# Performance work log

Hardware: AMD Instinct MI355X
Metric: run time of the kernel (lower is better)

The kernel has to match this reference:

```python
import jax, jax.numpy as jnp
import numpy as np

H = 8          # num_heads
EPS = 1e-6     # layernorm epsilon
NEG_INF = -1e9


def _ln(x, g, b):
    m = jnp.mean(x, axis=-1, keepdims=True)
    v = jnp.mean(jnp.square(x - m), axis=-1, keepdims=True)
    return g * (x - m) * jax.lax.rsqrt(v + EPS) + b


def _mha(xq, kv, wq, wk, wv, wo, bias):
    # xq: [B,Tq,D], kv: [B,Tk,D]; weights [D,D]. Returns (out [B,Tq,D], weights [B,H,Tq,Tk]).
    B, Tq, D = xq.shape
    dh = D // H
    q = (xq @ wq) * (dh ** -0.5)
    k = kv @ wk
    v = kv @ wv
    q = q.reshape(B, Tq, H, dh).transpose(0, 2, 1, 3)
    k = k.reshape(B, -1, H, dh).transpose(0, 2, 1, 3)
    v = v.reshape(B, -1, H, dh).transpose(0, 2, 1, 3)
    logits = jnp.einsum('bhqd,bhkd->bhqk', q, k)
    if bias is not None:
        logits = logits + bias
    w = jax.nn.softmax(logits, axis=-1)
    out = jnp.einsum('bhqk,bhkd->bhqd', w, v).transpose(0, 2, 1, 3).reshape(B, Tq, D)
    return out @ wo, w


def setup_inputs() -> dict:
    key = jax.random.key(0)
    ks = jax.random.split(key, 16)
    B, Td, Te, D, F, L = 2, 2048, 2048, 512, 2048, 2
    s = 0.02
    inp = {
        'x': jax.random.normal(ks[0], (B, Td, D), jnp.float32),
        'enc_a': jax.random.normal(ks[1], (B, Te, D), jnp.float32),
        'enc_c': jax.random.normal(ks[2], (B, Te, D), jnp.float32),
        'sa_wq': jax.random.normal(ks[3], (L, D, D), jnp.float32) * s,
        'sa_wk': jax.random.normal(ks[4], (L, D, D), jnp.float32) * s,
        'sa_wv': jax.random.normal(ks[5], (L, D, D), jnp.float32) * s,
        'sa_wo': jax.random.normal(ks[6], (L, D, D), jnp.float32) * s,
        'ed_wq': jax.random.normal(ks[7], (L, D, D), jnp.float32) * s,
        'ed_wk': jax.random.normal(ks[8], (L, D, D), jnp.float32) * s,
        'ed_wv': jax.random.normal(ks[9], (L, D, D), jnp.float32) * s,
        'ed_wo': jax.random.normal(ks[10], (L, D, D), jnp.float32) * s,
        'ffn_w1': jax.random.normal(ks[11], (L, D, F), jnp.float32) * s,
        'ffn_w2': jax.random.normal(ks[12], (L, F, D), jnp.float32) * s,
        'ln1_g': jnp.ones((L, D), jnp.float32), 'ln1_b': jnp.zeros((L, D), jnp.float32),
        'ln2_g': jnp.ones((L, D), jnp.float32), 'ln2_b': jnp.zeros((L, D), jnp.float32),
        'ln3_g': jnp.ones((L, D), jnp.float32), 'ln3_b': jnp.zeros((L, D), jnp.float32),
        'out_g': jnp.ones((D,), jnp.float32), 'out_b': jnp.zeros((D,), jnp.float32),
    }
    return inp


def reference(x, enc_a, enc_c, sa_wq, sa_wk, sa_wv, sa_wo, ed_wq, ed_wk, ed_wv, ed_wo,
              ffn_w1, ffn_w2, ln1_g, ln1_b, ln2_g, ln2_b, ln3_g, ln3_b, out_g, out_b):
    B, T, D = x.shape
    L = sa_wq.shape[0]
    # decoder self-attention causal bias, broadcast over [B,H]
    causal = jnp.where(jnp.tril(jnp.ones((T, T), bool)), 0.0, NEG_INF)[None, None]
    avg = None
    for i in range(L):
        h = _ln(x, ln1_g[i], ln1_b[i])
        y, _ = _mha(h, h, sa_wq[i], sa_wk[i], sa_wv[i], sa_wo[i], causal)
        x = x + y  # residual (dropout inactive at eval)
        h = _ln(x, ln2_g[i], ln2_b[i])
        y0, _ = _mha(h, enc_a, ed_wq[i], ed_wk[i], ed_wv[i], ed_wo[i], None)
        y1, w = _mha(h, enc_c, ed_wq[i], ed_wk[i], ed_wv[i], ed_wo[i], None)
        # original overwrites attn_scores with second call's head-averaged weights
        scores = jnp.mean(w, axis=1) / L
        avg = scores if avg is None else avg + scores
        x = x + y0 + y1
        h = _ln(x, ln3_g[i], ln3_b[i])
        x = x + jax.nn.relu(h @ ffn_w1[i]) @ ffn_w2[i]
    x = _ln(x, out_g, out_b)
    return x, avg
```

## Files before the change

kernel.cpp:

```cpp
#include <hip/hip_runtime.h>
#include <hip/hip_bf16.h>

#define BB 2
#define TT 2048
#define DD 512
#define FF 2048
#define HH 8
#define DH 64
#define LL 2
#define MM (BB*TT)

typedef __attribute__((ext_vector_type(8))) short bf16x8;
typedef __attribute__((ext_vector_type(4))) float f32x4;

__device__ __forceinline__ float bf2f(unsigned short u) {
    return __uint_as_float(((unsigned int)u) << 16);
}
__device__ __forceinline__ unsigned short f2bf(float f) {
    unsigned int u = __float_as_uint(f);
    u += 0x7fffu + ((u >> 16) & 1u);
    return (unsigned short)(u >> 16);
}
__device__ __forceinline__ unsigned int cvtpk(float a, float b) {
    unsigned int r;
    asm("v_cvt_pk_bf16_f32 %0, %1, %2" : "=v"(r) : "v"(a), "v"(b));
    return r;
}
__device__ __forceinline__ void gload16(const void* g, void* l) {
    __builtin_amdgcn_global_load_lds((__attribute__((address_space(1))) void*)g,
                                     (__attribute__((address_space(3))) void*)l, 16, 0, 0);
}

template<bool BF16OUT>
__global__ __launch_bounds__(256) void ln_kernel(const float* __restrict__ x,
                                                 const float* __restrict__ g,
                                                 const float* __restrict__ b,
                                                 void* __restrict__ out)
{
    const int row = blockIdx.x;
    const int tid = threadIdx.x;
    const float2 v = ((const float2*)(x + (size_t)row * DD))[tid];
    float s = v.x + v.y;
    float q = v.x * v.x + v.y * v.y;
    #pragma unroll
    for (int off = 32; off; off >>= 1) {
        s += __shfl_down(s, off);
        q += __shfl_down(q, off);
    }
    __shared__ float ss[4], qq[4];
    const int wid = tid >> 6;
    if ((tid & 63) == 0) { ss[wid] = s; qq[wid] = q; }
    __syncthreads();
    s = ss[0] + ss[1] + ss[2] + ss[3];
    q = qq[0] + qq[1] + qq[2] + qq[3];
    const float mean = s * (1.0f / DD);
    const float var = q * (1.0f / DD) - mean * mean;
    const float inv = rsqrtf(var + 1e-6f);
    const float2 gg = ((const float2*)g)[tid];
    const float2 bb = ((const float2*)b)[tid];
    const float ox = gg.x * (v.x - mean) * inv + bb.x;
    const float oy = gg.y * (v.y - mean) * inv + bb.y;
    if (BF16OUT) {
        const unsigned int pk = cvtpk(ox, oy);
        ((unsigned int*)((unsigned short*)out + (size_t)row * DD))[tid] = pk;
    } else {
        float2 o; o.x = ox; o.y = oy;
        ((float2*)((float*)out + (size_t)row * DD))[tid] = o;
    }
}

struct CvtEJob { const float* s; unsigned short* d; };
struct CvtEJobs2 { CvtEJob j[2]; };

__global__ __launch_bounds__(256) void cvt_kernel(CvtEJobs2 P, int n)
{
    const CvtEJob jb = P.j[blockIdx.z];
    const int i = (blockIdx.x * 256 + threadIdx.x) * 8;
    if (i >= n) return;
    const float4 a = *(const float4*)(jb.s + i);
    const float4 b = *(const float4*)(jb.s + i + 4);
    unsigned int o[4];
    o[0] = cvtpk(a.x, a.y); o[1] = cvtpk(a.z, a.w);
    o[2] = cvtpk(b.x, b.y); o[3] = cvtpk(b.z, b.w);
    *(bf16x8*)(jb.d + i) = *(bf16x8*)o;
}

struct CvtTJob { const float* s; unsigned short* d; int K; int N; };
struct CvtTJobs20 { CvtTJob j[20]; };

__global__ __launch_bounds__(256) void cvtT_kernel(CvtTJobs20 P)
{
    __shared__ float t[32][33];
    const CvtTJob jb = P.j[blockIdx.z];
    const int gk = blockIdx.y << 5, gn = blockIdx.x << 5;
    if (gk >= jb.K || gn >= jb.N) return;
    const int tx = threadIdx.x & 31, ty = threadIdx.x >> 5;
    #pragma unroll
    for (int i = 0; i < 4; ++i)
        t[ty + i * 8][tx] = jb.s[(size_t)(gk + ty + i * 8) * jb.N + gn + tx];
    __syncthreads();
    #pragma unroll
    for (int i = 0; i < 4; ++i)
        jb.d[(size_t)(gn + ty + i * 8) * jb.K + gk + tx] = f2bf(t[tx][ty + i * 8]);
}

struct GemmJob {
    const unsigned short* A;
    const unsigned short* Wt;
    const float* res;
    float* Cf;
    unsigned short* Cb;
    unsigned short* Ct;
    float scale;
    int relu;
};
struct GemmJobs8 { GemmJob j[8]; };

__global__ __launch_bounds__(256, 2) void gemm_mfma(GemmJobs8 P, int M, int N, int K)
{
    __shared__ __align__(16) unsigned char lds[32768];
    const GemmJob jb = P.j[blockIdx.z];
    const int tid = threadIdx.x, lane = tid & 63, w = tid >> 6;
    const int bn = blockIdx.x << 7, bm = blockIdx.y << 7;
    const int wr = (w >> 1) << 6, wc = (w & 1) << 6;
    const size_t strA = (size_t)K * 2;

    f32x4 acc[4][4] = {};
    const int akey = (lane & 7) << 4;
    const int frow = lane & 15;
    const int kq = (lane >> 4) << 4;

    for (int kt = 0; kt < K; kt += 64) {
        __syncthreads();
        #pragma unroll
        for (int c = 0; c < 4; ++c) {
            const int q = c * 4 + w;
            const int o = (q << 10) + (lane << 4);
            const int row = o >> 7;
            const int colb = (o & 127) ^ ((row & 7) << 4);
            gload16((const char*)jb.A + (size_t)(bm + row) * strA + kt * 2 + colb,
                    lds + (q << 10));
            gload16((const char*)jb.Wt + (size_t)(bn + row) * strA + kt * 2 + colb,
                    lds + 16384 + (q << 10));
        }
        asm volatile("s_waitcnt vmcnt(0)" ::: "memory");
        __syncthreads();
        #pragma unroll
        for (int kk = 0; kk < 2; ++kk) {
            bf16x8 av[4], bv[4];
            #pragma unroll
            for (int i = 0; i < 4; ++i) {
                const int rA = wr + (i << 4) + frow;
                av[i] = *(const bf16x8*)(lds + (rA << 7) + ((((kk << 6) + kq)) ^ akey));
                const int rB = wc + (i << 4) + frow;
                bv[i] = *(const bf16x8*)(lds + 16384 + (rB << 7) + ((((kk << 6) + kq)) ^ akey));
            }
            #pragma unroll
            for (int i = 0; i < 4; ++i)
                #pragma unroll
                for (int j = 0; j < 4; ++j)
                    acc[i][j] = __builtin_amdgcn_mfma_f32_16x16x32_bf16(av[i], bv[j], acc[i][j], 0, 0, 0);
        }
    }

    const int crow0 = (lane >> 4) << 2;
    const int ccol = lane & 15;
    if (jb.Ct) {
        #pragma unroll
        for (int i = 0; i < 4; ++i)
            #pragma unroll
            for (int j = 0; j < 4; ++j) {
                const int gm = bm + wr + (i << 4) + crow0;
                const int gn = bn + wc + (j << 4) + ccol;
                const int bI = gm >> 11, t = gm & 2047;
                const int hI = gn >> 6, d = gn & 63;
                uint2 pk;
                pk.x = cvtpk(acc[i][j][0], acc[i][j][1]);
                pk.y = cvtpk(acc[i][j][2], acc[i][j][3]);
                *(uint2*)(jb.Ct + ((size_t)((bI * HH + hI) * DH + d)) * TT + t) = pk;
            }
        return;
    }
    #pragma unroll
    for (int i = 0; i < 4; ++i) {
        #pragma unroll
        for (int j = 0; j < 4; ++j) {
            #pragma unroll
            for (int r = 0; r < 4; ++r) {
                const int gm = bm + wr + (i << 4) + crow0 + r;
                const int gn = bn + wc + (j << 4) + ccol;
                float v = acc[i][j][r] * jb.scale;
                if (jb.relu) v = fmaxf(v, 0.f);
                const size_t idx = (size_t)gm * N + gn;
                if (jb.res) v += jb.res[idx];
                if (jb.Cf) jb.Cf[idx] = v;
                if (jb.Cb) jb.Cb[idx] = f2bf(v);
            }
        }
    }
}

template<bool CAUSAL, bool DUAL, int NQ>
__global__ __launch_bounds__(256, (NQ == 1) ? 4 : 3) void flash_mfma(
    const unsigned short* __restrict__ q,
    const unsigned short* __restrict__ ka, const unsigned short* __restrict__ vta,
    const unsigned short* __restrict__ kc, const unsigned short* __restrict__ vtc,
    unsigned short* __restrict__ Opart,
    float* __restrict__ mlpart)
{
    __shared__ __align__(16) char lds[(NQ == 1) ? 40960 : 49152];
    const int tid = threadIdx.x;
    const int lane = tid & 63, w = tid >> 6;
    const int g4 = lane >> 4, c = lane & 15;

    constexpr int GX = (32 / NQ) * 2;
    const int f = blockIdx.x + GX * (blockIdx.y + 8 * blockIdx.z);
    const int xcd = f & 7;
    const int tt = f >> 3;
    const int u = tt % GX;
    const int half = u & 1, jq = u >> 1;
    const int grp = (tt / GX) * 8 + xcd;
    int b, h, which;
    if (DUAL) { which = grp & 1; b = (grp >> 1) & 1; h = grp >> 2; }
    else      { which = 0;       b = grp & 1;        h = grp >> 1; }
    const int q0 = jq * (64 * NQ);
    const int q0w = q0 + w * (16 * NQ);
    const int kendw = q0w + 16 * NQ;

    const unsigned short* k  = (DUAL && which) ? kc : ka;
    const unsigned short* vt = (DUAL && which) ? vtc : vta;
    const int slot = (DUAL ? (which << 1) : 0) + half;
    unsigned short* Od = Opart + (size_t)slot * MM * DD;
    float* mld = mlpart + (size_t)slot * (BB * HH * TT * 2);

    bf16x8 Qf[NQ][2];
    #pragma unroll
    for (int jb = 0; jb < NQ; ++jb) {
        const unsigned short* qp = q + (size_t)(b * TT + q0w + (jb << 4) + c) * DD + h * DH + (g4 << 3);
        Qf[jb][0] = *(const bf16x8*)qp;
        Qf[jb][1] = *(const bf16x8*)(qp + 32);
    }
    const char* kbase = (const char*)(k + (size_t)b * TT * DD + h * DH);
    const char* vtb   = (const char*)(vt + (size_t)(b * HH + h) * DH * TT);
    char* Pw = lds + 32768 + w * (NQ * 2048);
    const int pkey = (c & 7) << 4;

    f32x4 O[NQ][4] = {};
    float mval[NQ], lpart[NQ];
    #pragma unroll
    for (int jb = 0; jb < NQ; ++jb) { mval[jb] = -1e30f; lpart[jb] = 0.f; }

    const int ntt = CAUSAL ? ((q0 + 64 * NQ) >> 6) : (TT >> 6);
    const int tBeg = half ? ((ntt + 1) >> 1) : 0;
    const int tEnd = half ? ntt : ((ntt + 1) >> 1);

    auto STAGE = [&](int t, int sel) {
        const int kt = t << 6;
        char* Kb = lds + sel * 8192;
        char* Vb = lds + 16384 + sel * 8192;
        #pragma unroll
        for (int c8 = 0; c8 < 2; ++c8) {
            const int qc = (c8 << 2) + w;
            const int o = (qc << 10) + (lane << 4);
            const int row = o >> 7;
            const int colb = (o & 127) ^ ((row & 7) << 4);
            gload16(kbase + (size_t)(kt + row) * (DD * 2) + colb, Kb + (qc << 10));
            gload16(vtb + (size_t)row * (TT * 2) + kt * 2 + colb, Vb + (qc << 10));
        }
    };

    if (tBeg < tEnd) {
        STAGE(tBeg, 0);
        asm volatile("s_waitcnt vmcnt(0)" ::: "memory");
        __syncthreads();

        for (int t = tBeg; t < tEnd; ++t) {
            const int cur = (t - tBeg) & 1;
            if (t + 1 < tEnd) STAGE(t + 1, cur ^ 1);
            const int kt = t << 6;

            if (!CAUSAL || kt < kendw) {
                const char* Kb = lds + cur * 8192;
                const char* Vb = lds + 16384 + cur * 8192;

                f32x4 s[NQ][4] = {};
                #pragma unroll
                for (int kk = 0; kk < 2; ++kk) {
                    bf16x8 av[4];
                    #pragma unroll
                    for (int i = 0; i < 4; ++i) {
                        const int r = (i << 4) + c;
                        av[i] = *(const bf16x8*)(Kb + (r << 7) + (((kk << 6) + (g4 << 4)) ^ ((r & 7) << 4)));
                    }
                    #pragma unroll
                    for (int i = 0; i < 4; ++i)
                        #pragma unroll
                        for (int jb = 0; jb < NQ; ++jb)
                            s[jb][i] = __builtin_amdgcn_mfma_f32_16x16x32_bf16(av[i], Qf[jb][kk], s[jb][i], 0, 0, 0);
                }

                #pragma unroll
                for (int jb = 0; jb < NQ; ++jb) {
                    const int qbase = q0w + (jb << 4);
                    if (CAUSAL && kt + 63 > qbase) {
                        #pragma unroll
                        for (int i = 0; i < 4; ++i)
                            #pragma unroll
                            for (int r = 0; r < 4; ++r)
                                if (kt + (i << 4) + (g4 << 2) + r > qbase + c) s[jb][i][r] = -1e30f;
                    }
                    float pmax = -1e30f;
                    #pragma unroll
                    for (int i = 0; i < 4; ++i)
                        #pragma unroll
                        for (int r = 0; r < 4; ++r) pmax = fmaxf(pmax, s[jb][i][r]);
                    if (__any(pmax > mval[jb] + 11.f)) {
                        float mx = fmaxf(pmax, __shfl_xor(pmax, 16));
                        mx = fmaxf(mx, __shfl_xor(mx, 32));
                        const float mn = fmaxf(mval[jb], mx);
                        const float scf = exp2f(mval[jb] - mn);
                        lpart[jb] *= scf;
                        #pragma unroll
                        for (int r = 0; r < 4; ++r) {
                            const float fr = __shfl(scf, (g4 << 2) + r);
                            #pragma unroll
                            for (int jj = 0; jj < 4; ++jj) O[jb][jj][r] *= fr;
                        }
                        mval[jb] = mn;
                    }
                    float ps = 0.f;
                    #pragma unroll
                    for (int i = 0; i < 4; ++i)
                        #pragma unroll
                        for (int r = 0; r < 4; ++r) {
                            const float p = exp2f(s[jb][i][r] - mval[jb]);
                            s[jb][i][r] = p;
                            ps += p;
                        }
                    lpart[jb] += ps;
                    #pragma unroll
                    for (int i = 0; i < 4; ++i) {
                        uint2 pk;
                        pk.x = cvtpk(s[jb][i][0], s[jb][i][1]);
                        pk.y = cvtpk(s[jb][i][2], s[jb][i][3]);
                        const int baddr = (((jb << 4) + c) << 7) + (((i << 4) + (g4 << 2)) << 1);
                        *(uint2*)(Pw + (baddr ^ pkey)) = pk;
                    }
                }
                asm volatile("s_waitcnt lgkmcnt(0)" ::: "memory");
                __builtin_amdgcn_sched_barrier(0);

                #pragma unroll
                for (int kk = 0; kk < 2; ++kk) {
                    bf16x8 pa[NQ];
                    #pragma unroll
                    for (int jb = 0; jb < NQ; ++jb)
                        pa[jb] = *(const bf16x8*)(Pw + (((((jb << 4) + c) << 7) + (kk << 6) + (g4 << 4)) ^ pkey));
                    #pragma unroll
                    for (int jj = 0; jj < 4; ++jj) {
                        const int d = (jj << 4) + c;
                        const bf16x8 vb = *(const bf16x8*)(Vb + (d << 7) + (((kk << 6) + (g4 << 4)) ^ ((d & 7) << 4)));
                        #pragma unroll
                        for (int jb = 0; jb < NQ; ++jb)
                            O[jb][jj] = __builtin_amdgcn_mfma_f32_16x16x32_bf16(pa[jb], vb, O[jb][jj], 0, 0, 0);
                    }
                }
            }

            asm volatile("s_waitcnt vmcnt(0)" ::: "memory");
            __syncthreads();
        }
    }

    #pragma unroll
    for (int jb = 0; jb < NQ; ++jb) {
        float l2 = lpart[jb] + __shfl_xor(lpart[jb], 16);
        const float ltot = l2 + __shfl_xor(l2, 32);
        #pragma unroll
        for (int jj = 0; jj < 4; ++jj)
            #pragma unroll
            for (int r = 0; r < 4; ++r) {
                const int qr = q0w + (jb << 4) + (g4 << 2) + r;
                Od[(size_t)(b * TT + qr) * DD + h * DH + (jj << 4) + c] = f2bf(O[jb][jj][r]);
            }
        if (lane < 16) {
            const size_t mi = (((size_t)b * HH + h) * TT + q0w + (jb << 4) + lane) * 2;
            mld[mi] = mval[jb];
            mld[mi + 1] = ltot;
        }
    }
}

template<int NS>
__global__ __launch_bounds__(256) void merge_kernel(
    const unsigned short* __restrict__ Opart, const float* __restrict__ mlpart,
    unsigned short* __restrict__ out)
{
    const int row = blockIdx.x;
    const int b = row >> 11, rt = row & 2047;
    const int t = threadIdx.x;
    const int d0 = t << 1, h = d0 >> 6;
    float acc0 = 0.f, acc1 = 0.f;
    #pragma unroll
    for (int s = 0; s < NS; ++s) {
        const size_t mb = ((size_t)(b * HH + h) * TT + rt) * 2;
        const float* mp0 = mlpart + (size_t)(s * 2 + 0) * (BB * HH * TT * 2) + mb;
        const float* mp1 = mlpart + (size_t)(s * 2 + 1) * (BB * HH * TT * 2) + mb;
        const float m0 = mp0[0], l0 = mp0[1], m1 = mp1[0], l1 = mp1[1];
        const float M = fmaxf(m0, m1);
        const float a0 = exp2f(m0 - M), a1 = exp2f(m1 - M);
        const float inv = 1.f / (a0 * l0 + a1 * l1);
        const unsigned short* p0 = Opart + (size_t)(s * 2 + 0) * MM * DD + (size_t)row * DD + d0;
        const unsigned short* p1 = Opart + (size_t)(s * 2 + 1) * MM * DD + (size_t)row * DD + d0;
        acc0 += (a0 * bf2f(p0[0]) + a1 * bf2f(p1[0])) * inv;
        acc1 += (a0 * bf2f(p0[1]) + a1 * bf2f(p1[1])) * inv;
    }
    ((unsigned int*)(out + (size_t)row * DD))[t] = cvtpk(acc0, acc1);
}

__global__ __launch_bounds__(256) void avg_mfma_kernel(const unsigned short* __restrict__ qm,
                                                       const unsigned short* __restrict__ kcm,
                                                       const float* __restrict__ mlpart,
                                                       float* __restrict__ avg, int first)
{
    __shared__ __align__(16) unsigned char ldsQ[2][8192];
    __shared__ __align__(16) unsigned char ldsK[2][8192];
    const int tid = threadIdx.x;
    const int lane = tid & 63, w = tid >> 6;
    const int g4 = lane >> 4, c = lane & 15;
    const int kt0 = blockIdx.x << 6, q0 = blockIdx.y << 6, b = blockIdx.z;
    const int qrow = q0 + (w << 4) + c;

    float m8[8], il8[8];
    #pragma unroll
    for (int h = 0; h < 8; ++h) {
        const size_t mb = ((size_t)(b * HH + h) * TT + qrow) * 2;
        const float* mp2 = mlpart + (size_t)2 * (BB * HH * TT * 2) + mb;
        const float* mp3 = mlpart + (size_t)3 * (BB * HH * TT * 2) + mb;
        const float m2 = mp2[0], l2v = mp2[1], m3 = mp3[0], l3v = mp3[1];
        const float M = fmaxf(m2, m3);
        const float L = exp2f(m2 - M) * l2v + exp2f(m3 - M) * l3v;
        m8[h] = M;
        il8[h] = 1.f / L;
    }

    auto STAGE = [&](int h, int sel) {
        #pragma unroll
        for (int u2 = 0; u2 < 2; ++u2) {
            const int qc = (u2 << 2) + w;
            const int o = (qc << 10) + (lane << 4);
            const int row = o >> 7;
            const int colb = (o & 127) ^ ((row & 7) << 4);
            gload16((const char*)qm + ((size_t)(b * TT + q0 + row) * DD + h * DH) * 2 + colb,
                    &ldsQ[sel][qc << 10]);
            gload16((const char*)kcm + ((size_t)(b * TT + kt0 + row) * DD + h * DH) * 2 + colb,
                    &ldsK[sel][qc << 10]);
        }
    };

    f32x4 avac[4] = {};
    STAGE(0, 0);
    asm volatile("s_waitcnt vmcnt(0)" ::: "memory");
    __syncthreads();

    for (int h = 0; h < 8; ++h) {
        const int cur = h & 1;
        if (h + 1 < 8) STAGE(h + 1, cur ^ 1);
        f32x4 s[4] = {};
        #pragma unroll
        for (int kk = 0; kk < 2; ++kk) {
            const int qrl = (w << 4) + c;
            const bf16x8 qf = *(const bf16x8*)(&ldsQ[cur][(qrl << 7) + (((kk << 6) + (g4 << 4)) ^ ((qrl & 7) << 4))]);
            #pragma unroll
            for (int i = 0; i < 4; ++i) {
                const int r = (i << 4) + c;
                const bf16x8 av = *(const bf16x8*)(&ldsK[cur][(r << 7) + (((kk << 6) + (g4 << 4)) ^ ((r & 7) << 4))]);
                s[i] = __builtin_amdgcn_mfma_f32_16x16x32_bf16(av, qf, s[i], 0, 0, 0);
            }
        }
        #pragma unroll
        for (int i = 0; i < 4; ++i)
            #pragma unroll
            for (int r = 0; r < 4; ++r)
                avac[i][r] += exp2f(s[i][r] - m8[h]) * il8[h];
        asm volatile("s_waitcnt vmcnt(0)" ::: "memory");
        __syncthreads();
    }

    float* dst = avg + (size_t)(b * TT + qrow) * TT + kt0;
    #pragma unroll
    for (int i = 0; i < 4; ++i) {
        const int kc = (i << 4) + (g4 << 2);
        float4 vv;
        vv.x = avac[i][0] * (1.f / (HH * LL));
        vv.y = avac[i][1] * (1.f / (HH * LL));
        vv.z = avac[i][2] * (1.f / (HH * LL));
        vv.w = avac[i][3] * (1.f / (HH * LL));
        float4* p = (float4*)(dst + kc);
        if (first) {
            *p = vv;
        } else {
            float4 old = *p;
            old.x += vv.x; old.y += vv.y; old.z += vv.z; old.w += vv.w;
            *p = old;
        }
    }
}

extern "C" void kernel_launch(void* const* d_in, const int* in_sizes, int n_in,
                              void* d_out, int out_size, void* d_ws, size_t ws_size,
                              hipStream_t stream)
{
    const float* x_in   = (const float*)d_in[0];
    const float* enc_a  = (const float*)d_in[1];
    const float* enc_c  = (const float*)d_in[2];
    const float* sa_wq0 = (const float*)d_in[3];
    const float* sa_wk0 = (const float*)d_in[4];
    const float* sa_wv0 = (const float*)d_in[5];
    const float* sa_wo0 = (const float*)d_in[6];
    const float* ed_wq0 = (const float*)d_in[7];
    const float* ed_wk0 = (const float*)d_in[8];
    const float* ed_wv0 = (const float*)d_in[9];
    const float* ed_wo0 = (const float*)d_in[10];
    const float* ffn_w10 = (const float*)d_in[11];
    const float* ffn_w20 = (const float*)d_in[12];
    const float* ln1_g0 = (const float*)d_in[13];
    const float* ln1_b0 = (const float*)d_in[14];
    const float* ln2_g0 = (const float*)d_in[15];
    const float* ln2_b0 = (const float*)d_in[16];
    const float* ln3_g0 = (const float*)d_in[17];
    const float* ln3_b0 = (const float*)d_in[18];
    const float* out_g  = (const float*)d_in[19];
    const float* out_b  = (const float*)d_in[20];

    const size_t NTD = (size_t)MM * DD;
    const size_t MB = 1u << 20;
    char* W = (char*)d_ws;
    float*          x_buf   = (float*)(W);
    unsigned short* h_bf    = (unsigned short*)(W + 8 * MB);
    unsigned short* q_bf    = (unsigned short*)(W + 12 * MB);
    unsigned short* k1_bf   = (unsigned short*)(W + 16 * MB);
    unsigned short* vt1     = (unsigned short*)(W + 20 * MB);
    unsigned short* k2_bf   = (unsigned short*)(W + 24 * MB);
    unsigned short* vt2     = (unsigned short*)(W + 28 * MB);
    unsigned short* attnA   = (unsigned short*)(W + 32 * MB);
    unsigned short* attnS   = (unsigned short*)(W + 36 * MB);
    unsigned short* encA_bf = (unsigned short*)(W + 41 * MB);
    unsigned short* encC_bf = (unsigned short*)(W + 45 * MB);
    unsigned short* wbf     = (unsigned short*)(W + 49 * MB);
    unsigned short* Opart   = (unsigned short*)(W + 68 * MB);
    float*          mlpart  = (float*)(W + 84 * MB);
    unsigned short* ffn_bf  = q_bf;

    const bool fused = (ws_size >= (size_t)97 * MB);
    unsigned short* k1c  = fused ? (unsigned short*)(W + 88 * MB) : k1_bf;
    unsigned short* vt1c = fused ? (unsigned short*)(W + 92 * MB) : vt1;

    unsigned short* w1t = wbf + (size_t)16 * DD * DD;
    unsigned short* w2t = w1t + (size_t)2 * DD * FF;
    auto wd = [&](int l, int which) { return wbf + ((size_t)(l * 8 + which)) * DD * DD; };

    float* x_out   = (float*)d_out;
    float* avg_out = (float*)d_out + NTD;

    hipMemcpyAsync(x_buf, x_in, NTD * sizeof(float), hipMemcpyDeviceToDevice, stream);

    {
        CvtTJobs20 J{};
        const float* srcs[8] = {sa_wq0, sa_wk0, sa_wv0, sa_wo0, ed_wq0, ed_wk0, ed_wv0, ed_wo0};
        for (int l = 0; l < LL; ++l)
            for (int t = 0; t < 8; ++t)
                J.j[l * 8 + t] = {srcs[t] + (size_t)l * DD * DD, wd(l, t), DD, DD};
        for (int l = 0; l < LL; ++l) {
            J.j[16 + l] = {ffn_w10 + (size_t)l * DD * FF, w1t + (size_t)l * FF * DD, DD, FF};
            J.j[18 + l] = {ffn_w20 + (size_t)l * FF * DD, w2t + (size_t)l * DD * FF, FF, DD};
        }
        cvtT_kernel<<<dim3(FF / 32, FF / 32, 20), 256, 0, stream>>>(J);
    }
    {
        CvtEJobs2 J{};
        J.j[0] = {enc_a, encA_bf};
        J.j[1] = {enc_c, encC_bf};
        cvt_kernel<<<dim3(NTD / 8 / 256, 1, 2), 256, 0, stream>>>(J, (int)NTD);
    }

    const dim3 flashSelfG(64, HH, BB);
    const dim3 flashCrossG(32, HH, BB * 2);
    const dim3 avgG(TT / 64, TT / 64, BB);
    const float qscale = 0.125f * 1.4426950408889634f;

    for (int i = 0; i < LL; ++i) {
        const size_t fOff = (size_t)i * DD * FF;
        const size_t lOff = (size_t)i * DD;

        ln_kernel<true><<<MM, 256, 0, stream>>>(x_buf, ln1_g0 + lOff, ln1_b0 + lOff, h_bf);
        if (fused) {
            GemmJobs8 J{};
            J.j[0] = {h_bf,    wd(i, 0), nullptr, nullptr, q_bf, nullptr, qscale, 0};
            J.j[1] = {h_bf,    wd(i, 1), nullptr, nullptr, k1_bf, nullptr, 1.f, 0};
            J.j[2] = {h_bf,    wd(i, 2), nullptr, nullptr, nullptr, vt1, 1.f, 0};
            J.j[3] = {encA_bf, wd(i, 5), nullptr, nullptr, k1c, nullptr, 1.f, 0};
            J.j[4] = {encA_bf, wd(i, 6), nullptr, nullptr, nullptr, vt1c, 1.f, 0};
            J.j[5] = {encC_bf, wd(i, 5), nullptr, nullptr, k2_bf, nullptr, 1.f, 0};
            J.j[6] = {encC_bf, wd(i, 6), nullptr, nullptr, nullptr, vt2, 1.f, 0};
            gemm_mfma<<<dim3(DD / 128, MM / 128, 7), 256, 0, stream>>>(J, MM, DD, DD);
        } else {
            GemmJobs8 J{};
            J.j[0] = {h_bf, wd(i, 0), nullptr, nullptr, q_bf, nullptr, qscale, 0};
            J.j[1] = {h_bf, wd(i, 1), nullptr, nullptr, k1_bf, nullptr, 1.f, 0};
            J.j[2] = {h_bf, wd(i, 2), nullptr, nullptr, nullptr, vt1, 1.f, 0};
            gemm_mfma<<<dim3(DD / 128, MM / 128, 3), 256, 0, stream>>>(J, MM, DD, DD);
        }
        flash_mfma<true, false, 1><<<flashSelfG, 256, 0, stream>>>(
            q_bf, k1_bf, vt1, nullptr, nullptr, Opart, mlpart);
        merge_kernel<1><<<MM, 256, 0, stream>>>(Opart, mlpart, attnA);
        {
            GemmJobs8 J{};
            J.j[0] = {attnA, wd(i, 3), x_buf, x_buf, nullptr, nullptr, 1.f, 0};
            gemm_mfma<<<dim3(DD / 128, MM / 128, 1), 256, 0, stream>>>(J, MM, DD, DD);
        }

        ln_kernel<true><<<MM, 256, 0, stream>>>(x_buf, ln2_g0 + lOff, ln2_b0 + lOff, h_bf);
        if (fused) {
            GemmJobs8 J{};
            J.j[0] = {h_bf, wd(i, 4), nullptr, nullptr, q_bf, nullptr, qscale, 0};
            gemm_mfma<<<dim3(DD / 128, MM / 128, 1), 256, 0, stream>>>(J, MM, DD, DD);
        } else {
            GemmJobs8 J{};
            J.j[0] = {h_bf,    wd(i, 4), nullptr, nullptr, q_bf, nullptr, qscale, 0};
            J.j[1] = {encA_bf, wd(i, 5), nullptr, nullptr, k1_bf, nullptr, 1.f, 0};
            J.j[2] = {encA_bf, wd(i, 6), nullptr, nullptr, nullptr, vt1, 1.f, 0};
            J.j[3] = {encC_bf, wd(i, 5), nullptr, nullptr, k2_bf, nullptr, 1.f, 0};
            J.j[4] = {encC_bf, wd(i, 6), nullptr, nullptr, nullptr, vt2, 1.f, 0};
            gemm_mfma<<<dim3(DD / 128, MM / 128, 5), 256, 0, stream>>>(J, MM, DD, DD);
        }
        flash_mfma<false, true, 2><<<flashCrossG, 256, 0, stream>>>(
            q_bf, k1c, vt1c, k2_bf, vt2, Opart, mlpart);
        merge_kernel<2><<<MM, 256, 0, stream>>>(Opart, mlpart, attnS);
        avg_mfma_kernel<<<avgG, 256, 0, stream>>>(q_bf, k2_bf, mlpart, avg_out, (i == 0) ? 1 : 0);
        {
            GemmJobs8 J{};
            J.j[0] = {attnS, wd(i, 7), x_buf, x_buf, nullptr, nullptr, 1.f, 0};
            gemm_mfma<<<dim3(DD / 128, MM / 128, 1), 256, 0, stream>>>(J, MM, DD, DD);
        }

        ln_kernel<true><<<MM, 256, 0, stream>>>(x_buf, ln3_g0 + lOff, ln3_b0 + lOff, h_bf);
        {
            GemmJobs8 J{};
            J.j[0] = {h_bf, w1t + fOff, nullptr, nullptr, ffn_bf, nullptr, 1.f, 1};
            gemm_mfma<<<dim3(FF / 128, MM / 128, 1), 256, 0, stream>>>(J, MM, FF, DD);
        }
        {
            GemmJobs8 J{};
            J.j[0] = {ffn_bf, w2t + fOff, x_buf, x_buf, nullptr, nullptr, 1.f, 0};
            gemm_mfma<<<dim3(DD / 128, MM / 128, 1), 256, 0, stream>>>(J, MM, DD, FF);
        }
    }

    ln_kernel<false><<<MM, 256, 0, stream>>>(x_buf, out_g, out_b, x_out);
}
```

Baseline: 727.6 us.

## Rework avg-score kernel to single-wave 64x64 tiles with XCD-aware block mapping

The head-averaged attention-weight kernel now uses one 64-lane wave per block that computes a full 64x64 tile of 16 MFMA outputs, reusing Q and K fragments across a 4x4 register block instead of four waves each doing a 16-row strip. Block indices are remapped so each XCD handles a contiguous batch and query range, aiming for better L2 locality. Per-row max and inverse-sum stats move to LDS, and the pipelining uses a partial vmcnt wait instead of full waits plus block barriers. The risks are higher register pressure from 64 accumulators plus 64 scores, lower occupancy, and output stores that are now scalar and less coalesced (16 consecutive floats per row).

```diff
diff --git a/kernel.cpp b/kernel.cpp
--- a/kernel.cpp
+++ b/kernel.cpp
@@ -418,93 +418,107 @@
     ((unsigned int*)(out + (size_t)row * DD))[t] = cvtpk(acc0, acc1);
 }
 
-__global__ __launch_bounds__(256) void avg_mfma_kernel(const unsigned short* __restrict__ qm,
-                                                       const unsigned short* __restrict__ kcm,
-                                                       const float* __restrict__ mlpart,
-                                                       float* __restrict__ avg, int first)
+__global__ __launch_bounds__(64) void avg_mfma_kernel(const unsigned short* __restrict__ qm,
+                                                      const unsigned short* __restrict__ kcm,
+                                                      const float* __restrict__ mlpart,
+                                                      float* __restrict__ avg, int first)
 {
     __shared__ __align__(16) unsigned char ldsQ[2][8192];
     __shared__ __align__(16) unsigned char ldsK[2][8192];
-    const int tid = threadIdx.x;
-    const int lane = tid & 63, w = tid >> 6;
-    const int g4 = lane >> 4, c = lane & 15;
-    const int kt0 = blockIdx.x << 6, q0 = blockIdx.y << 6, b = blockIdx.z;
-    const int qrow = q0 + (w << 4) + c;
-
-    float m8[8], il8[8];
+    __shared__ float sM[8][64];
+    __shared__ float sIL[8][64];
+    const int lane = threadIdx.x;
+
+    const int f = blockIdx.x + 32 * (blockIdx.y + 32 * blockIdx.z);
+    const int xcd = f & 7, t = f >> 3;
+    const int b = xcd >> 2;
+    const int q0 = (((xcd & 3) << 3) + (t >> 5)) << 6;
+    const int kt0 = (t & 31) << 6;
+
     #pragma unroll
     for (int h = 0; h < 8; ++h) {
-        const size_t mb = ((size_t)(b * HH + h) * TT + qrow) * 2;
+        const size_t mb = ((size_t)(b * HH + h) * TT + q0 + lane) * 2;
         const float* mp2 = mlpart + (size_t)2 * (BB * HH * TT * 2) + mb;
         const float* mp3 = mlpart + (size_t)3 * (BB * HH * TT * 2) + mb;
         const float m2 = mp2[0], l2v = mp2[1], m3 = mp3[0], l3v = mp3[1];
         const float M = fmaxf(m2, m3);
         const float L = exp2f(m2 - M) * l2v + exp2f(m3 - M) * l3v;
-        m8[h] = M;
-        il8[h] = 1.f / L;
-    }
+        sM[h][lane] = M;
+        sIL[h][lane] = 1.f / L;
+    }
+
+    float avac[4][4][4] = {};
+    const int akey = (lane & 7) << 4;
+    const int frow = lane & 15;
+    const int kq = (lane >> 4) << 4;
+    const int crow0 = (lane >> 4) << 2;
 
     auto STAGE = [&](int h, int sel) {
         #pragma unroll
-        for (int u2 = 0; u2 < 2; ++u2) {
-            const int qc = (u2 << 2) + w;
-            const int o = (qc << 10) + (lane << 4);
+        for (int c = 0; c < 8; ++c) {
+            const int o = (c << 10) + (lane << 4);
             const int row = o >> 7;
             const int colb = (o & 127) ^ ((row & 7) << 4);
             gload16((const char*)qm + ((size_t)(b * TT + q0 + row) * DD + h * DH) * 2 + colb,
-                    &ldsQ[sel][qc << 10]);
+                    &ldsQ[sel][c << 10]);
             gload16((const char*)kcm + ((size_t)(b * TT + kt0 + row) * DD + h * DH) * 2 + colb,
-                    &ldsK[sel][qc << 10]);
+                    &ldsK[sel][c << 10]);
         }
     };
 
-    f32x4 avac[4] = {};
+    asm volatile("s_waitcnt vmcnt(0)" ::: "memory");
     STAGE(0, 0);
-    asm volatile("s_waitcnt vmcnt(0)" ::: "memory");
-    __syncthreads();
 
     for (int h = 0; h < 8; ++h) {
         const int cur = h & 1;
-        if (h + 1 < 8) STAGE(h + 1, cur ^ 1);
-        f32x4 s[4] = {};
+        if (h < 7) {
+            STAGE(h + 1, cur ^ 1);
+            asm volatile("s_waitcnt vmcnt(16)" ::: "memory");
+        } else {
+            asm volatile("s_waitcnt vmcnt(0)" ::: "memory");
+        }
+        __builtin_amdgcn_sched_barrier(0);
+
+        f32x4 s[4][4] = {};
         #pragma unroll
         for (int kk = 0; kk < 2; ++kk) {
-            const int qrl = (w << 4) + c;
-            const bf16x8 qf = *(const bf16x8*)(&ldsQ[cur][(qrl << 7) + (((kk << 6) + (g4 << 4)) ^ ((qrl & 7) << 4))]);
+            bf16x8 qv[4], kv[4];
             #pragma unroll
             for (int i = 0; i < 4; ++i) {
-                const int r = (i << 4) + c;
-                const bf16x8 av = *(const bf16x8*)(&ldsK[cur][(r << 7) + (((kk << 6) + (g4 << 4)) ^ ((r & 7) << 4))]);
-                s[i] = __builtin_amdgcn_mfma_f32_16x16x32_bf16(av, qf, s[i], 0, 0, 0);
+                qv[i] = *(const bf16x8*)(&ldsQ[cur][(((i << 4) + frow) << 7) + (((kk << 6) + kq) ^ akey)]);
+                kv[i] = *(const bf16x8*)(&ldsK[cur][(((i << 4) + frow) << 7) + (((kk << 6) + kq) ^ akey)]);
             }
+            #pragma unroll
+            for (int i = 0; i < 4; ++i)
+                #pragma unroll
+                for (int j = 0; j < 4; ++j)
+                    s[i][j] = __builtin_amdgcn_mfma_f32_16x16x32_bf16(qv[i], kv[j], s[i][j], 0, 0, 0);
         }
         #pragma unroll
         for (int i = 0; i < 4; ++i)
             #pragma unroll
-            for (int r = 0; r < 4; ++r)
-                avac[i][r] += exp2f(s[i][r] - m8[h]) * il8[h];
-        asm volatile("s_waitcnt vmcnt(0)" ::: "memory");
-        __syncthreads();
-    }
-
-    float* dst = avg + (size_t)(b * TT + qrow) * TT + kt0;
-    #pragma unroll
-    for (int i = 0; i < 4; ++i) {
-        const int kc = (i << 4) + (g4 << 2);
-        float4 vv;
-        vv.x = avac[i][0] * (1.f / (HH * LL));
-        vv.y = avac[i][1] * (1.f / (HH * LL));
-        vv.z = avac[i][2] * (1.f / (HH * LL));
-        vv.w = avac[i][3] * (1.f / (HH * LL));
-        float4* p = (float4*)(dst + kc);
-        if (first) {
-            *p = vv;
-        } else {
-            float4 old = *p;
-            old.x += vv.x; old.y += vv.y; old.z += vv.z; old.w += vv.w;
-            *p = old;
-        }
-    }
+            for (int j = 0; j < 4; ++j)
+                #pragma unroll
+                for (int r = 0; r < 4; ++r) {
+                    const int qr = (i << 4) + crow0 + r;
+                    avac[i][j][r] += exp2f(s[i][j][r] - sM[h][qr]) * sIL[h][qr];
+                }
+        __builtin_amdgcn_sched_barrier(0);
+    }
+
+    float* dst = avg + ((size_t)b * TT + q0) * TT + kt0;
+    #pragma unroll
+    for (int i = 0; i < 4; ++i)
+        #pragma unroll
+        for (int j = 0; j < 4; ++j)
+            #pragma unroll
+            for (int r = 0; r < 4; ++r) {
+                const int qr = (i << 4) + crow0 + r;
+                const int kc = (j << 4) + (lane & 15);
+                const float v = avac[i][j][r] * (1.f / (HH * LL));
+                float* p = dst + (size_t)qr * TT + kc;
+                *p = first ? v : (*p + v);
+            }
 }
 
 extern "C" void kernel_launch(void* const* d_in, const int* in_sizes, int n_in,
@@ -637,7 +651,7 @@
         flash_mfma<false, true, 2><<<flashCrossG, 256, 0, stream>>>(
             q_bf, k1c, vt1c, k2_bf, vt2, Opart, mlpart);
         merge_kernel<2><<<MM, 256, 0, stream>>>(Opart, mlpart, attnS);
-        avg_mfma_kernel<<<avgG, 256, 0, stream>>>(q_bf, k2_bf, mlpart, avg_out, (i == 0) ? 1 : 0);
+        avg_mfma_kernel<<<avgG, 64, 0, stream>>>(q_bf, k2_bf, mlpart, avg_out, (i == 0) ? 1 : 0);
         {
             GemmJobs8 J{};
             J.j[0] = {attnS, wd(i, 7), x_buf, x_buf, nullptr, nullptr, 1.f, 0};
```

After: 688.1 us. 5.4% less time.
